# Kernel tuning notes

Measured on AMD Instinct MI355X. Metric: run time of the kernel, lower is better.

Reference implementation:

```python
import jax, jax.numpy as jnp
import numpy as np

BLOCK = 32  # ggml quant block size


def setup_inputs() -> dict:
    key = jax.random.key(0)
    k1, k2, k3, k4 = jax.random.split(key, 4)
    IN, OUT = 8192, 8192
    x = jax.random.normal(k1, (2, 8, IN), dtype=jnp.float32)
    # quantized codes in [0, 255), centered by -127 at dequant time
    qweight = jax.random.randint(k2, (OUT, IN), 0, 255, dtype=jnp.int32)
    # per-block scales, small positive values like real ggml d
    scales = jax.random.uniform(k3, (OUT, IN // BLOCK), dtype=jnp.float32) * 0.01
    bias = jax.random.normal(k4, (OUT,), dtype=jnp.float32)
    return {"x": x, "qweight": qweight, "scales": scales, "bias": bias}


def reference(x, qweight, scales, bias):
    OUT, IN = qweight.shape
    # dequantize: centered int codes * per-block scale -> [OUT, IN]
    w = (qweight.astype(jnp.float32) - 127.0).reshape(OUT, IN // BLOCK, BLOCK)
    w = (w * scales[:, :, None]).reshape(OUT, IN)
    xf = x.reshape(-1, IN)                     # [T, IN]
    out = xf @ w.T + bias                      # [T, OUT]
    return out.reshape(*x.shape[:-1], OUT)
```

## Files before the change

### kernel.cpp

```cpp
#include <hip/hip_runtime.h>
#include <stdint.h>

#define INF 8192
#define OUTF 8192
#define TOK 16
#define KSPLIT 8
#define KR (INF / KSPLIT)
#define ROWS_PER_BLOCK 64
#define LDS_STRIDE (KR + 8)

typedef __attribute__((ext_vector_type(8))) short short8;
typedef __attribute__((ext_vector_type(4))) short short4v;
typedef __attribute__((ext_vector_type(4))) float float4v;
typedef __attribute__((ext_vector_type(4))) int int4v;

__device__ __forceinline__ short f2bf(float f) {
    uint32_t u = __builtin_bit_cast(uint32_t, f);
    u += 0x7fffu + ((u >> 16) & 1u);
    return (short)(u >> 16);
}

__device__ __forceinline__ void stage_x(const float* __restrict__ x, short* xs,
                                        int k0, int tid) {
    #pragma unroll
    for (int it = 0; it < (TOK * KR / 4) / 256; ++it) {
        int idx = tid + it * 256;
        int t  = idx >> 8;
        int kq = idx & 255;
        float4v xv = *reinterpret_cast<const float4v*>(x + (size_t)t * INF + k0 + kq * 4);
        short4v h;
        h[0] = f2bf(xv[0]); h[1] = f2bf(xv[1]); h[2] = f2bf(xv[2]); h[3] = f2bf(xv[3]);
        *reinterpret_cast<short4v*>(xs + t * LDS_STRIDE + kq * 4) = h;
    }
}

__device__ __forceinline__ float4v kloop(const short* xs,
                                         const int* __restrict__ qrow,
                                         const float* __restrict__ srow,
                                         int lane, float4v acc) {
    int col = lane & 15;
    int kg  = lane >> 4;
    const short* aptr = xs + col * LDS_STRIDE + kg * 8;

    int4v qa = *reinterpret_cast<const int4v*>(qrow);
    int4v qb = *reinterpret_cast<const int4v*>(qrow + 4);
    float s  = srow[0];

    #pragma unroll 4
    for (int i = 0; i < KR / 32; ++i) {
        int ip = (i < KR / 32 - 1) ? i + 1 : i;
        int4v na = *reinterpret_cast<const int4v*>(qrow + ip * 32);
        int4v nb = *reinterpret_cast<const int4v*>(qrow + ip * 32 + 4);
        float ns = srow[ip];

        float m = -127.0f * s;
        short8 bfrag;
        bfrag[0] = f2bf(fmaf((float)qa[0], s, m));
        bfrag[1] = f2bf(fmaf((float)qa[1], s, m));
        bfrag[2] = f2bf(fmaf((float)qa[2], s, m));
        bfrag[3] = f2bf(fmaf((float)qa[3], s, m));
        bfrag[4] = f2bf(fmaf((float)qb[0], s, m));
        bfrag[5] = f2bf(fmaf((float)qb[1], s, m));
        bfrag[6] = f2bf(fmaf((float)qb[2], s, m));
        bfrag[7] = f2bf(fmaf((float)qb[3], s, m));

        short8 afrag = *reinterpret_cast<const short8*>(aptr + i * 32);

        acc = __builtin_amdgcn_mfma_f32_16x16x32_bf16(afrag, bfrag, acc, 0, 0, 0);

        qa = na; qb = nb; s = ns;
    }
    return acc;
}

__global__ __launch_bounds__(256, 4) void gemm_q8_part(
    const float* __restrict__ x, const int* __restrict__ qw,
    const float* __restrict__ scales, float* __restrict__ pbuf)
{
    __shared__ short xs[TOK * LDS_STRIDE];
    int rg = blockIdx.x >> 3;
    int ks = blockIdx.x & 7;
    int k0 = ks * KR;
    int tid = threadIdx.x;

    stage_x(x, xs, k0, tid);
    __syncthreads();

    int wave = tid >> 6;
    int lane = tid & 63;
    int col  = lane & 15;
    int kg   = lane >> 4;
    int r0 = rg * ROWS_PER_BLOCK + wave * 16;
    int r  = r0 + col;

    const int*   qrow = qw + (size_t)r * INF + k0 + kg * 8;
    const float* srow = scales + (size_t)r * (INF / 32) + (k0 >> 5);

    float4v acc = {0.f, 0.f, 0.f, 0.f};
    acc = kloop(xs, qrow, srow, lane, acc);

    float* pb = pbuf + (size_t)ks * TOK * OUTF;
    #pragma unroll
    for (int i = 0; i < 4; ++i) {
        int t = kg * 4 + i;
        pb[(size_t)t * OUTF + r0 + col] = acc[i];
    }
}

__global__ __launch_bounds__(256) void reduce_bias_k(
    const float* __restrict__ pbuf, const float* __restrict__ bias,
    float* __restrict__ out)
{
    int gid = blockIdx.x * 256 + threadIdx.x;
    int f = gid * 4;
    int t = f >> 13;
    int r = f & (OUTF - 1);
    float4v a = *reinterpret_cast<const float4v*>(bias + r);
    #pragma unroll
    for (int s = 0; s < KSPLIT; ++s) {
        float4v p = *reinterpret_cast<const float4v*>(pbuf + (size_t)(s * TOK + t) * OUTF + r);
        a += p;
    }
    *reinterpret_cast<float4v*>(out + f) = a;
}

__global__ __launch_bounds__(256, 4) void gemm_q8_direct(
    const float* __restrict__ x, const int* __restrict__ qw,
    const float* __restrict__ scales, const float* __restrict__ bias,
    float* __restrict__ out)
{
    __shared__ short xs[TOK * LDS_STRIDE];
    int rg = blockIdx.x;
    int tid = threadIdx.x;
    int wave = tid >> 6;
    int lane = tid & 63;
    int col  = lane & 15;
    int kg   = lane >> 4;
    int r0 = rg * ROWS_PER_BLOCK + wave * 16;
    int r  = r0 + col;

    float4v acc = {0.f, 0.f, 0.f, 0.f};
    for (int ks = 0; ks < KSPLIT; ++ks) {
        int k0 = ks * KR;
        __syncthreads();
        stage_x(x, xs, k0, tid);
        __syncthreads();
        const int*   qrow = qw + (size_t)r * INF + k0 + kg * 8;
        const float* srow = scales + (size_t)r * (INF / 32) + (k0 >> 5);
        acc = kloop(xs, qrow, srow, lane, acc);
    }
    #pragma unroll
    for (int i = 0; i < 4; ++i) {
        int t = kg * 4 + i;
        out[(size_t)t * OUTF + r0 + col] = acc[i] + bias[r0 + col];
    }
}

extern "C" void kernel_launch(void* const* d_in, const int* in_sizes, int n_in,
                              void* d_out, int out_size, void* d_ws, size_t ws_size,
                              hipStream_t stream) {
    const float* x      = (const float*)d_in[0];
    const int*   qw     = (const int*)d_in[1];
    const float* scales = (const float*)d_in[2];
    const float* bias   = (const float*)d_in[3];
    float* out = (float*)d_out;

    size_t need = (size_t)KSPLIT * TOK * OUTF * sizeof(float);
    if (ws_size >= need) {
        float* pbuf = (float*)d_ws;
        gemm_q8_part<<<(OUTF / ROWS_PER_BLOCK) * KSPLIT, 256, 0, stream>>>(x, qw, scales, pbuf);
        reduce_bias_k<<<(TOK * OUTF / 4) / 256, 256, 0, stream>>>(pbuf, bias, out);
    } else {
        gemm_q8_direct<<<OUTF / ROWS_PER_BLOCK, 256, 0, stream>>>(x, qw, scales, bias, out);
    }
}
```

Baseline: 56.37 us.

## Deepen weight prefetch, use nontemporal loads, and cheapen bf16 packing

The weight and scale loads in the dequant K-loop now go two iterations ahead instead of one, and they use nontemporal loads because the streamed int32 weights are read only once. The bf16 conversion switches from round-to-nearest-even per element to a cheaper round-half-up that packs two values at once. This cuts VALU work per MFMA and should hide more memory latency, at the cost of extra registers that may lower occupancy and a slightly different rounding result.

New measurement: 79.50 us. +41.0%, slower.

```diff
diff --git a/kernel.cpp b/kernel.cpp
--- a/kernel.cpp
+++ b/kernel.cpp
@@ -6,6 +6,7 @@
 #define TOK 16
 #define KSPLIT 8
 #define KR (INF / KSPLIT)
+#define NI (KR / 32)
 #define ROWS_PER_BLOCK 64
 #define LDS_STRIDE (KR + 8)
 
@@ -13,11 +14,22 @@
 typedef __attribute__((ext_vector_type(4))) short short4v;
 typedef __attribute__((ext_vector_type(4))) float float4v;
 typedef __attribute__((ext_vector_type(4))) int int4v;
+typedef __attribute__((ext_vector_type(4))) uint32_t uint4v;
 
 __device__ __forceinline__ short f2bf(float f) {
     uint32_t u = __builtin_bit_cast(uint32_t, f);
     u += 0x7fffu + ((u >> 16) & 1u);
     return (short)(u >> 16);
+}
+
+__device__ __forceinline__ uint32_t pkbf(float a, float b) {
+    uint32_t ua = __builtin_bit_cast(uint32_t, a) + 0x8000u;
+    uint32_t ub = __builtin_bit_cast(uint32_t, b) + 0x8000u;
+    return (ua >> 16) | (ub & 0xffff0000u);
+}
+
+__device__ __forceinline__ int4v ntl(const int* p) {
+    return __builtin_nontemporal_load(reinterpret_cast<const int4v*>(p));
 }
 
 __device__ __forceinline__ void stage_x(const float* __restrict__ x, short* xs,
@@ -42,33 +54,40 @@
     int kg  = lane >> 4;
     const short* aptr = xs + col * LDS_STRIDE + kg * 8;
 
-    int4v qa = *reinterpret_cast<const int4v*>(qrow);
-    int4v qb = *reinterpret_cast<const int4v*>(qrow + 4);
-    float s  = srow[0];
+    int4v A0 = ntl(qrow);          int4v B0 = ntl(qrow + 4);
+    int4v A1 = ntl(qrow + 32);     int4v B1 = ntl(qrow + 36);
+    float s0 = srow[0], s1 = srow[1];
 
     #pragma unroll 4
-    for (int i = 0; i < KR / 32; ++i) {
-        int ip = (i < KR / 32 - 1) ? i + 1 : i;
-        int4v na = *reinterpret_cast<const int4v*>(qrow + ip * 32);
-        int4v nb = *reinterpret_cast<const int4v*>(qrow + ip * 32 + 4);
-        float ns = srow[ip];
+    for (int i = 0; i < NI; ++i) {
+        int ip = (i + 2 < NI) ? (i + 2) : (NI - 1);
+        int4v A2 = ntl(qrow + ip * 32);
+        int4v B2 = ntl(qrow + ip * 32 + 4);
+        float s2 = __builtin_nontemporal_load(srow + ip);
 
-        float m = -127.0f * s;
-        short8 bfrag;
-        bfrag[0] = f2bf(fmaf((float)qa[0], s, m));
-        bfrag[1] = f2bf(fmaf((float)qa[1], s, m));
-        bfrag[2] = f2bf(fmaf((float)qa[2], s, m));
-        bfrag[3] = f2bf(fmaf((float)qa[3], s, m));
-        bfrag[4] = f2bf(fmaf((float)qb[0], s, m));
-        bfrag[5] = f2bf(fmaf((float)qb[1], s, m));
-        bfrag[6] = f2bf(fmaf((float)qb[2], s, m));
-        bfrag[7] = f2bf(fmaf((float)qb[3], s, m));
+        float m = -127.0f * s0;
+        float f0 = fmaf((float)A0[0], s0, m);
+        float f1 = fmaf((float)A0[1], s0, m);
+        float f2 = fmaf((float)A0[2], s0, m);
+        float f3 = fmaf((float)A0[3], s0, m);
+        float f4 = fmaf((float)B0[0], s0, m);
+        float f5 = fmaf((float)B0[1], s0, m);
+        float f6 = fmaf((float)B0[2], s0, m);
+        float f7 = fmaf((float)B0[3], s0, m);
+
+        uint4v pk;
+        pk[0] = pkbf(f0, f1);
+        pk[1] = pkbf(f2, f3);
+        pk[2] = pkbf(f4, f5);
+        pk[3] = pkbf(f6, f7);
+        short8 bfrag = __builtin_bit_cast(short8, pk);
 
         short8 afrag = *reinterpret_cast<const short8*>(aptr + i * 32);
 
         acc = __builtin_amdgcn_mfma_f32_16x16x32_bf16(afrag, bfrag, acc, 0, 0, 0);
 
-        qa = na; qb = nb; s = ns;
+        A0 = A1; B0 = B1; s0 = s1;
+        A1 = A2; B1 = B2; s1 = s2;
     }
     return acc;
 }
```
